# Kernel tuning notes

Hardware: AMD Instinct MI355X
Metric: run time of the kernel (lower is better)

## Reference

```python
import jax, jax.numpy as jnp
import numpy as np

IN_DIMS = 4
DEPTH = 4
C = IN_DIMS + 1                     # channels after time augmentation
SIG = sum(C ** k for k in range(1, DEPTH + 1))  # 780
N, T = 64, 1024


def setup_inputs() -> dict:
    key = jax.random.key(0)
    k1, k2, k3, k4, k5 = jax.random.split(key, 5)
    batch = jax.random.normal(k1, (N, T, IN_DIMS), dtype=jnp.float32)
    s_c = 1.0 / np.sqrt(C)
    conv_w = jax.random.normal(k2, (C, C), dtype=jnp.float32) * s_c
    conv_b = jax.random.normal(k3, (C,), dtype=jnp.float32) * s_c
    s_l = 1.0 / np.sqrt(SIG)
    lin_w = jax.random.normal(k4, (SIG, SIG), dtype=jnp.float32) * s_l
    lin_b = jax.random.normal(k5, (SIG,), dtype=jnp.float32) * s_l
    return {"batch": batch, "conv_w": conv_w, "conv_b": conv_b,
            "lin_w": lin_w, "lin_b": lin_b}


def _stream_signature(path):
    """Streamed path signature with zero basepoint.

    path: (n, t, C). Returns (n, t, SIG) where entry t is the signature of
    the piecewise-linear path (0, path[0], ..., path[t]) truncated at DEPTH,
    levels flattened in lexicographic (row-major) order like signatory.
    """
    n = path.shape[0]
    # increments; basepoint=True means first increment is path[:,0] - 0
    dx = jnp.concatenate([path[:, :1, :], path[:, 1:, :] - path[:, :-1, :]], axis=1)
    init = tuple(jnp.zeros((n, C ** k), path.dtype) for k in range(1, DEPTH + 1))

    def step(levels, d):
        # exp(d) in the truncated tensor algebra: e_k = d^{(x)k} / k!
        e = [d]
        for k in range(2, DEPTH + 1):
            e.append((jnp.einsum('na,nb->nab', e[-1], d) / k).reshape(n, -1))
        # Chen: new_k = e_k + S_k + sum_{i=1}^{k-1} S_i (x) e_{k-i}
        new = []
        for k in range(1, DEPTH + 1):
            acc = levels[k - 1] + e[k - 1]
            for i in range(1, k):
                acc = acc + jnp.einsum('na,nb->nab', levels[i - 1], e[k - i - 1]).reshape(n, -1)
            new.append(acc)
        new = tuple(new)
        return new, jnp.concatenate(new, axis=-1)

    _, ys = jax.lax.scan(step, init, jnp.swapaxes(dx, 0, 1))  # ys: (t, n, SIG)
    return jnp.swapaxes(ys, 0, 1)


def reference(batch, conv_w, conv_b, lin_w, lin_b):
    n, t, _ = batch.shape
    # time augmentation: append channel arange(1,T+1)/T
    time = (jnp.arange(1, t + 1, dtype=batch.dtype) / t)[None, :, None]
    a = jnp.concatenate([batch, jnp.broadcast_to(time, (n, t, 1))], axis=-1)  # (n,t,C)
    # kernel-size-1 conv1d == pointwise linear over channels
    b = a @ conv_w.T + conv_b                                                  # (n,t,C)
    c = _stream_signature(b)                                                   # (n,t,SIG)
    # zero out the first stream entry (torch.concat of zeros with c[:,1:,:])
    c = jnp.concatenate([jnp.zeros((n, 1, SIG), c.dtype), c[:, 1:, :]], axis=1)
    return jnp.tanh(c @ lin_w.T + lin_b)
```

## Files before the change

### kernel.cpp

```cpp
#include <hip/hip_runtime.h>
#include <math.h>

#define N_B 64
#define T_LEN 1024
#define IN_D 4
#define CH 5
#define SIG 780
#define KP 800
#define SEG_LEN 16
#define N_SEG 64
#define SC_L1 1.0f
#define SC_L2 0.25f
#define SC_L3 0.0625f
#define SC_L4 0.015625f

typedef _Float16 f16x8 __attribute__((ext_vector_type(8)));
typedef float f32x4 __attribute__((ext_vector_type(4)));

typedef __attribute__((address_space(1))) const void* as1cp;
typedef __attribute__((address_space(3))) void* as3p;

#define VMCNT(n) asm volatile("s_waitcnt vmcnt(" #n ")" ::: "memory")

__device__ __forceinline__ float fast_tanh(float x) {
  float ax = fabsf(x);
  float e = __expf(-2.0f * ax);
  float r = (1.0f - e) * __builtin_amdgcn_rcpf(1.0f + e);
  return copysignf(r, x);
}

__global__ __launch_bounds__(256) void conv_kernel(
    const float* __restrict__ batch,
    const float* __restrict__ conv_w,
    const float* __restrict__ conv_b,
    float* __restrict__ b_out) {
  int idx = blockIdx.x * blockDim.x + threadIdx.x;
  if (idx >= N_B * T_LEN) return;
  int t = idx & (T_LEN - 1);
  const float* a = batch + (size_t)idx * IN_D;
  float a0 = a[0], a1 = a[1], a2 = a[2], a3 = a[3];
  float tm = (float)(t + 1) / (float)T_LEN;
  float* o = b_out + (size_t)idx * CH;
#pragma unroll
  for (int j = 0; j < CH; ++j) {
    const float* w = conv_w + j * CH;
    float r = conv_b[j];
    r = fmaf(tm, w[4], r);
    r = fmaf(a3, w[3], r);
    r = fmaf(a2, w[2], r);
    r = fmaf(a1, w[1], r);
    r = fmaf(a0, w[0], r);
    o[j] = r;
  }
}

__global__ __launch_bounds__(320) void seg_kernel(
    const float* __restrict__ batch,
    const float* __restrict__ conv_w,
    const float* __restrict__ conv_b,
    float* __restrict__ P) {
  int s = blockIdx.x;
  int n = blockIdx.y;
  int tid = threadIdx.x;

  __shared__ float S[2][SIG];
  __shared__ float bc[(SEG_LEN + 1) * CH];
  __shared__ float dsh[SEG_LEN][CH];

  for (int i = tid; i < SIG; i += 320) S[0][i] = 0.0f;
  if (tid < (SEG_LEN + 1) * CH) {
    int r = s * SEG_LEN - 1 + tid / CH, ch = tid % CH;
    float v = 0.0f;
    if (r >= 0) {
      const float* a = batch + ((size_t)n * T_LEN + r) * IN_D;
      const float* w = conv_w + ch * CH;
      v = conv_b[ch];
      v = fmaf(a[0], w[0], v);
      v = fmaf(a[1], w[1], v);
      v = fmaf(a[2], w[2], v);
      v = fmaf(a[3], w[3], v);
      v = fmaf((float)(r + 1) * (1.0f / T_LEN), w[4], v);
    }
    bc[tid] = v;
  }
  __syncthreads();
  if (tid < SEG_LEN * CH) {
    int j = tid / CH, ch = tid % CH;
    dsh[j][ch] = bc[(j + 1) * CH + ch] - bc[j * CH + ch];
  }

  const int x0 = tid;
  const int x1 = tid + 320;
  const bool has1 = (tid < 305);
  const int a0i = x0 / 125, b0i = (x0 / 25) % 5, c0i = (x0 / 5) % 5, d0i = x0 % 5;
  const int a1i = x1 / 125, b1i = (x1 / 25) % 5, c1i = (x1 / 5) % 5, d1i = x1 % 5;
  const int s2_0 = x0 / 25, s3_0 = x0 / 5;
  const int s2_1 = x1 / 25, s3_1 = x1 / 5;
  const bool hasL3 = (tid < 125);
  const int ya = tid / 25, yb = (tid / 5) % 5, yc = tid % 5;
  const bool hasL2 = (tid < 25);
  const int za = tid / 5, zb = tid % 5;
  const bool hasL1 = (tid < CH);
  __syncthreads();

  int c = 0;
  for (int j = 0; j < SEG_LEN; ++j) {
    const float* Sc = S[c];
    float* Sn = S[c ^ 1];
    float n4_0, n4_1 = 0.0f, n3 = 0.0f, n2 = 0.0f, n1 = 0.0f;
    {
      float tH = fmaf(0.25f, dsh[j][a0i], Sc[a0i]);
      tH = fmaf((1.0f / 3.0f) * dsh[j][b0i], tH, Sc[5 + s2_0]);
      tH = fmaf(0.5f * dsh[j][c0i], tH, Sc[30 + s3_0]);
      n4_0 = fmaf(dsh[j][d0i], tH, Sc[155 + x0]);
    }
    if (has1) {
      float tH = fmaf(0.25f, dsh[j][a1i], Sc[a1i]);
      tH = fmaf((1.0f / 3.0f) * dsh[j][b1i], tH, Sc[5 + s2_1]);
      tH = fmaf(0.5f * dsh[j][c1i], tH, Sc[30 + s3_1]);
      n4_1 = fmaf(dsh[j][d1i], tH, Sc[155 + x1]);
    }
    if (hasL3) {
      float tH = fmaf((1.0f / 3.0f), dsh[j][ya], Sc[ya]);
      tH = fmaf(0.5f * dsh[j][yb], tH, Sc[5 + ya * 5 + yb]);
      n3 = fmaf(dsh[j][yc], tH, Sc[30 + tid]);
    }
    if (hasL2) {
      float tH = fmaf(0.5f, dsh[j][za], Sc[za]);
      n2 = fmaf(dsh[j][zb], tH, Sc[5 + tid]);
    }
    if (hasL1) n1 = Sc[tid] + dsh[j][tid];
    Sn[155 + x0] = n4_0;
    if (has1) Sn[155 + x1] = n4_1;
    if (hasL3) Sn[30 + tid] = n3;
    if (hasL2) Sn[5 + tid] = n2;
    if (hasL1) Sn[tid] = n1;
    __syncthreads();
    c ^= 1;
  }

  float* Pr = P + ((size_t)n * N_SEG + s) * SIG;
  for (int i = tid; i < SIG; i += 320) Pr[i] = S[c][i];
}

__global__ __launch_bounds__(640) void prefix_kernel(float* __restrict__ P) {
  int n = blockIdx.x;
  int tid = threadIdx.x;
  __shared__ float A[2][SIG];
  __shared__ float Bs[SIG];

  float* Pn = P + (size_t)n * N_SEG * SIG;
  for (int i = tid; i < SIG; i += 640) A[0][i] = Pn[i];
  int i0 = tid, i1 = tid + 640;
  float r0 = 0.f, r1 = 0.f;
  if (i0 < SIG) r0 = Pn[SIG + i0];
  if (i1 < SIG) r1 = Pn[SIG + i1];

  const int e4 = tid;
  const int q4a = e4 / 125, r125 = e4 % 125, r25 = e4 % 25, r5 = e4 % 5;
  const int e4d5 = e4 / 5, e4d25 = e4 / 25;
  const int e3 = tid;
  const int e3a = e3 / 25, e3r25 = e3 % 25, e3r5 = e3 % 5, e3d5 = e3 / 5;
  const int e2 = tid - 125;
  const int e1 = tid - 150;

  int c = 0;
  for (int s = 1; s < N_SEG; ++s) {
    if (i0 < SIG) Bs[i0] = r0;
    if (i1 < SIG) Bs[i1] = r1;
    __syncthreads();
    if (s + 1 < N_SEG) {
      const float* Pnx = Pn + (size_t)(s + 1) * SIG;
      if (i0 < SIG) r0 = Pnx[i0];
      if (i1 < SIG) r1 = Pnx[i1];
    }
    const float* Ac = A[c];
    float* An = A[c ^ 1];
    float* Po = Pn + (size_t)s * SIG;
    if (tid < 625) {
      float v4 = Ac[155 + e4] + Bs[155 + e4];
      v4 = fmaf(Ac[30 + e4d5], Bs[r5], v4);
      v4 = fmaf(Ac[5 + e4d25], Bs[5 + r25], v4);
      v4 = fmaf(Ac[q4a], Bs[30 + r125], v4);
      An[155 + e4] = v4; Po[155 + e4] = v4;
    }
    if (tid < 125) {
      float v3 = Ac[30 + e3] + Bs[30 + e3];
      v3 = fmaf(Ac[5 + e3d5], Bs[e3r5], v3);
      v3 = fmaf(Ac[e3a], Bs[5 + e3r25], v3);
      An[30 + e3] = v3; Po[30 + e3] = v3;
    } else if (tid < 150) {
      float v2 = Ac[5 + e2] + Bs[5 + e2];
      v2 = fmaf(Ac[e2 / 5], Bs[e2 % 5], v2);
      An[5 + e2] = v2; Po[5 + e2] = v2;
    } else if (tid < 155) {
      float v1 = Ac[e1] + Bs[e1];
      An[e1] = v1; Po[e1] = v1;
    }
    c ^= 1;
  }
}

__global__ __launch_bounds__(320) void emit_kernel(
    const float* __restrict__ batch,
    const float* __restrict__ conv_w,
    const float* __restrict__ conv_b,
    const float* __restrict__ P,
    _Float16* __restrict__ c1,
    _Float16* __restrict__ c2) {
  int s = blockIdx.x;
  int n = blockIdx.y;
  int tid = threadIdx.x;

  __shared__ float S[2][SIG];
  __shared__ float bc[(SEG_LEN + 1) * CH];
  __shared__ float dsh[SEG_LEN][CH];
  __shared__ __align__(16) _Float16 row1[2][KP];
  __shared__ __align__(16) _Float16 row2[2][KP];

  if (s == 0) {
    for (int i = tid; i < SIG; i += 320) S[0][i] = 0.0f;
  } else {
    const float* Pr = P + ((size_t)n * N_SEG + (s - 1)) * SIG;
    for (int i = tid; i < SIG; i += 320) S[0][i] = Pr[i];
  }
  if (tid < (SEG_LEN + 1) * CH) {
    int r = s * SEG_LEN - 1 + tid / CH, ch = tid % CH;
    float v = 0.0f;
    if (r >= 0) {
      const float* a = batch + ((size_t)n * T_LEN + r) * IN_D;
      const float* w = conv_w + ch * CH;
      v = conv_b[ch];
      v = fmaf(a[0], w[0], v);
      v = fmaf(a[1], w[1], v);
      v = fmaf(a[2], w[2], v);
      v = fmaf(a[3], w[3], v);
      v = fmaf((float)(r + 1) * (1.0f / T_LEN), w[4], v);
    }
    bc[tid] = v;
  }
  if (tid < KP - SIG) {
    row1[0][SIG + tid] = (_Float16)0.0f;
    row1[1][SIG + tid] = (_Float16)0.0f;
    row2[0][SIG + tid] = (_Float16)0.0f;
    row2[1][SIG + tid] = (_Float16)0.0f;
  }
  __syncthreads();
  if (tid < SEG_LEN * CH) {
    int j = tid / CH, ch = tid % CH;
    dsh[j][ch] = bc[(j + 1) * CH + ch] - bc[j * CH + ch];
  }

  const int x0 = tid;
  const int x1 = tid + 320;
  const bool has1 = (tid < 305);
  const int a0i = x0 / 125, b0i = (x0 / 25) % 5, c0i = (x0 / 5) % 5, d0i = x0 % 5;
  const int a1i = x1 / 125, b1i = (x1 / 25) % 5, c1i = (x1 / 5) % 5, d1i = x1 % 5;
  const int s2_0 = x0 / 25, s3_0 = x0 / 5;
  const int s2_1 = x1 / 25, s3_1 = x1 / 5;
  const bool hasL3 = (tid < 125);
  const int ya = tid / 25, yb = (tid / 5) % 5, yc = tid % 5;
  const bool hasL2 = (tid < 25);
  const int za = tid / 5, zb = tid % 5;
  const bool hasL1 = (tid < CH);
  __syncthreads();

  int c = 0;
  for (int j = 0; j < SEG_LEN; ++j) {
    int t = s * SEG_LEN + j;
    const float* Sc = S[c];
    float* Sn = S[c ^ 1];
    float n4_0, n4_1 = 0.0f, n3 = 0.0f, n2 = 0.0f, n1 = 0.0f;
    {
      float tH = fmaf(0.25f, dsh[j][a0i], Sc[a0i]);
      tH = fmaf((1.0f / 3.0f) * dsh[j][b0i], tH, Sc[5 + s2_0]);
      tH = fmaf(0.5f * dsh[j][c0i], tH, Sc[30 + s3_0]);
      n4_0 = fmaf(dsh[j][d0i], tH, Sc[155 + x0]);
    }
    if (has1) {
      float tH = fmaf(0.25f, dsh[j][a1i], Sc[a1i]);
      tH = fmaf((1.0f / 3.0f) * dsh[j][b1i], tH, Sc[5 + s2_1]);
      tH = fmaf(0.5f * dsh[j][c1i], tH, Sc[30 + s3_1]);
      n4_1 = fmaf(dsh[j][d1i], tH, Sc[155 + x1]);
    }
    if (hasL3) {
      float tH = fmaf((1.0f / 3.0f), dsh[j][ya], Sc[ya]);
      tH = fmaf(0.5f * dsh[j][yb], tH, Sc[5 + ya * 5 + yb]);
      n3 = fmaf(dsh[j][yc], tH, Sc[30 + tid]);
    }
    if (hasL2) {
      float tH = fmaf(0.5f, dsh[j][za], Sc[za]);
      n2 = fmaf(dsh[j][zb], tH, Sc[5 + tid]);
    }
    if (hasL1) n1 = Sc[tid] + dsh[j][tid];

    if (j > 0) {
      size_t base = ((size_t)n * T_LEN + (t - 1)) * KP;
      if (tid < 100) {
        *(float4*)(c1 + base + tid * 8) = *(const float4*)&row1[c][tid * 8];
      } else if (tid < 200) {
        int cc = tid - 100;
        *(float4*)(c2 + base + cc * 8) = *(const float4*)&row2[c][cc * 8];
      }
    }

    Sn[155 + x0] = n4_0;
    if (has1) Sn[155 + x1] = n4_1;
    if (hasL3) Sn[30 + tid] = n3;
    if (hasL2) Sn[5 + tid] = n2;
    if (hasL1) Sn[tid] = n1;

    float z = (t == 0) ? 0.0f : 1.0f;
    {
      float v = n4_0 * SC_L4 * z;
      _Float16 h = (_Float16)v;
      row1[c ^ 1][155 + x0] = h; row2[c ^ 1][155 + x0] = (_Float16)(v - (float)h);
    }
    if (has1) {
      float v = n4_1 * SC_L4 * z;
      _Float16 h = (_Float16)v;
      row1[c ^ 1][155 + x1] = h; row2[c ^ 1][155 + x1] = (_Float16)(v - (float)h);
    }
    if (hasL3) {
      float v = n3 * SC_L3 * z;
      _Float16 h = (_Float16)v;
      row1[c ^ 1][30 + tid] = h; row2[c ^ 1][30 + tid] = (_Float16)(v - (float)h);
    }
    if (hasL2) {
      float v = n2 * SC_L2 * z;
      _Float16 h = (_Float16)v;
      row1[c ^ 1][5 + tid] = h; row2[c ^ 1][5 + tid] = (_Float16)(v - (float)h);
    }
    if (hasL1) {
      float v = n1 * SC_L1 * z;
      _Float16 h = (_Float16)v;
      row1[c ^ 1][tid] = h; row2[c ^ 1][tid] = (_Float16)(v - (float)h);
    }
    __syncthreads();
    c ^= 1;
  }
  {
    size_t base = ((size_t)n * T_LEN + (s * SEG_LEN + SEG_LEN - 1)) * KP;
    if (tid < 100) {
      *(float4*)(c1 + base + tid * 8) = *(const float4*)&row1[c][tid * 8];
    } else if (tid < 200) {
      int cc = tid - 100;
      *(float4*)(c2 + base + cc * 8) = *(const float4*)&row2[c][cc * 8];
    }
  }
}

__global__ __launch_bounds__(256) void wconv_kernel(
    const float* __restrict__ W,
    _Float16* __restrict__ w1,
    _Float16* __restrict__ w2) {
  int idx = blockIdx.x * blockDim.x + threadIdx.x;
  if (idx >= 896 * KP) return;
  int nn = idx / KP, k = idx % KP;
  float v = 0.0f;
  if (nn < SIG && k < SIG) {
    float sc = (k < 5) ? 1.0f : (k < 30) ? 4.0f : (k < 155) ? 16.0f : 64.0f;
    v = W[(size_t)nn * SIG + k] * sc;
  }
  _Float16 h = (_Float16)v;
  w1[idx] = h;
  w2[idx] = (_Float16)(v - (float)h);
}

__global__ __launch_bounds__(512, 2) void gemm_mfma(
    const _Float16* __restrict__ A1p, const _Float16* __restrict__ A2p,
    const _Float16* __restrict__ B1p, const _Float16* __restrict__ B2p,
    const float* __restrict__ bias, float* __restrict__ out) {
  __shared__ _Float16 Al[3][2][256 * 32];
  __shared__ _Float16 Bl[3][2][128 * 32];

  int tid = threadIdx.x;
  int lane = tid & 63, wid = tid >> 6;
  int wm = wid >> 1, wn = wid & 1;

  int b = blockIdx.x;
  int xcd = b & 7, sidx = b >> 3;
  int mt = (sidx / 7) * 8 + xcd;
  int nt = sidx % 7;
  int m0 = mt * 256;
  int n0 = nt * 128;

  f32x4 acc[4][4];
#pragma unroll
  for (int i = 0; i < 4; ++i)
#pragma unroll
    for (int j = 0; j < 4; ++j) acc[i][j] = (f32x4){0.f, 0.f, 0.f, 0.f};

  int sr = lane >> 2, scn = lane & 3;
  int swst = (sr ^ (sr >> 2)) & 3;
  int qg = scn ^ swst;
  int fr = lane & 15, fq = lane >> 4;
  int swf = (fr ^ (fr >> 2)) & 3;
  int fchunk = fq ^ swf;

  auto stageA = [&](int kb, int buf, int i) {
    int k0 = kb * 32;
    int linear = wid * 4 + i;
    int plane = linear >> 4, grp = linear & 15;
    size_t g = (size_t)(m0 + grp * 16 + sr) * KP + k0 + qg * 8;
    const _Float16* src = (plane ? A2p : A1p) + g;
    __builtin_amdgcn_global_load_lds((as1cp)src, (as3p)(&Al[buf][plane][grp * 512]), 16, 0, 0);
  };
  auto stageB = [&](int kb, int buf, int i) {
    int k0 = kb * 32;
    int linear = wid * 2 + i;
    int plane = linear >> 3, grp = linear & 7;
    size_t g = (size_t)(n0 + grp * 16 + sr) * KP + k0 + qg * 8;
    const _Float16* src = (plane ? B2p : B1p) + g;
    __builtin_amdgcn_global_load_lds((as1cp)src, (as3p)(&Bl[buf][plane][grp * 512]), 16, 0, 0);
  };

#pragma unroll
  for (int i = 0; i < 4; ++i) stageA(0, 0, i);
#pragma unroll
  for (int i = 0; i < 2; ++i) stageB(0, 0, i);
#pragma unroll
  for (int i = 0; i < 4; ++i) stageA(1, 1, i);
#pragma unroll
  for (int i = 0; i < 2; ++i) stageB(1, 1, i);

  int cur = 0;
#pragma unroll 1
  for (int kb = 0; kb < 25; ++kb) {
    int nx = cur + 2; if (nx >= 3) nx -= 3;
    bool pf = (kb + 2 < 25);
    if (kb < 24) { VMCNT(6); } else { VMCNT(0); }
    __builtin_amdgcn_s_barrier();
    __builtin_amdgcn_sched_barrier(0);
    f16x8 a1f[4], a2f[4], b1f[4], b2f[4];
    {
      int off = (wn * 64 + 0 * 16 + fr) * 32 + fchunk * 8;
      b1f[0] = *(const f16x8*)&Bl[cur][0][off];
      b2f[0] = *(const f16x8*)&Bl[cur][1][off];
    }
#pragma unroll
    for (int tm = 0; tm < 4; ++tm) {
      int off = (wm * 64 + tm * 16 + fr) * 32 + fchunk * 8;
      a1f[tm] = *(const f16x8*)&Al[cur][0][off];
      a2f[tm] = *(const f16x8*)&Al[cur][1][off];
    }
#pragma unroll
    for (int tn = 1; tn < 4; ++tn) {
      int off = (wn * 64 + tn * 16 + fr) * 32 + fchunk * 8;
      b1f[tn] = *(const f16x8*)&Bl[cur][0][off];
      b2f[tn] = *(const f16x8*)&Bl[cur][1][off];
    }
    if (pf) {
      stageA(kb + 2, nx, 0); stageA(kb + 2, nx, 1);
      stageA(kb + 2, nx, 2); stageA(kb + 2, nx, 3);
      stageB(kb + 2, nx, 0); stageB(kb + 2, nx, 1);
    }
#pragma unroll
    for (int tn = 0; tn < 4; ++tn) {
#pragma unroll
      for (int tm = 0; tm < 4; ++tm) {
        acc[tm][tn] = __builtin_amdgcn_mfma_f32_16x16x32_f16(a1f[tm], b1f[tn], acc[tm][tn], 0, 0, 0);
        acc[tm][tn] = __builtin_amdgcn_mfma_f32_16x16x32_f16(a1f[tm], b2f[tn], acc[tm][tn], 0, 0, 0);
        acc[tm][tn] = __builtin_amdgcn_mfma_f32_16x16x32_f16(a2f[tm], b1f[tn], acc[tm][tn], 0, 0, 0);
      }
    }
    cur = cur + 1; if (cur >= 3) cur -= 3;
  }
  __syncthreads();

  float* ep = (float*)(&Al[0][0][0]) + wid * 2112;

  float bv[4];
#pragma unroll
  for (int tn = 0; tn < 4; ++tn) {
    int nn = n0 + wn * 64 + tn * 16 + fr;
    bv[tn] = (nn < SIG) ? bias[nn] : 0.0f;
  }
#pragma unroll
  for (int h = 0; h < 2; ++h) {
#pragma unroll
    for (int tm2 = 0; tm2 < 2; ++tm2) {
      int tm = h * 2 + tm2;
#pragma unroll
      for (int tn = 0; tn < 4; ++tn) {
#pragma unroll
        for (int r = 0; r < 4; ++r) {
          int lr = tm2 * 16 + fq * 4 + r;
          int lc = tn * 16 + fr;
          ep[lr * 66 + lc] = fast_tanh(acc[tm][tn][r] + bv[tn]);
        }
      }
    }
#pragma unroll
    for (int p = 0; p < 2; ++p) {
      int lr = lane & 31;
      int ck = (lane >> 5) * 2 + p;
      int gm = m0 + wm * 64 + h * 32 + lr;
      int gc0 = n0 + wn * 64 + ck * 16;
#pragma unroll
      for (int q = 0; q < 4; ++q) {
        int col = gc0 + q * 4;
        if (col + 3 < SIG) {
          *(float4*)(out + (size_t)gm * SIG + col) =
              *(const float4*)&ep[lr * 66 + ck * 16 + q * 4];
        } else if (col < SIG) {
#pragma unroll
          for (int e = 0; e < 4; ++e) {
            int c2 = col + e;
            if (c2 < SIG) out[(size_t)gm * SIG + c2] = ep[lr * 66 + ck * 16 + q * 4 + e];
          }
        }
      }
    }
  }
}

__global__ __launch_bounds__(320) void sig_kernel_fb(
    const float* __restrict__ b_in, float* __restrict__ c_out) {
  int n = blockIdx.x;
  int tid = threadIdx.x;
  __shared__ float S[SIG];
  __shared__ float bc[64 * CH];
  __shared__ float dsh[CH];
  __shared__ float pb[CH];
  for (int i = tid; i < SIG; i += 320) S[i] = 0.0f;
  if (tid < CH) pb[tid] = 0.0f;
  const float* bn = b_in + (size_t)n * T_LEN * CH;
  float* cn = c_out + (size_t)n * T_LEN * SIG;
  const int x0 = tid, x1 = tid + 320;
  const bool has1 = (tid < 305);
  const int a0i = x0 / 125, b0i = (x0 / 25) % 5, c0i = (x0 / 5) % 5, d0i = x0 % 5;
  const int a1i = x1 / 125, b1i = (x1 / 25) % 5, c1i = (x1 / 5) % 5, d1i = x1 % 5;
  const int s2_0 = x0 / 25, s3_0 = x0 / 5, s2_1 = x1 / 25, s3_1 = x1 / 5;
  const bool hasL3 = (tid < 125);
  const int ya = tid / 25, yb = (tid / 5) % 5, yc = tid % 5;
  const bool hasL2 = (tid < 25);
  const int za = tid / 5, zb = tid % 5;
  const bool hasL1 = (tid < CH);
  for (int t = 0; t < T_LEN; ++t) {
    if ((t & 63) == 0) {
      __syncthreads();
      bc[tid] = bn[t * CH + tid];
      __syncthreads();
    }
    if (tid < CH) {
      float cur = bc[(t & 63) * CH + tid];
      dsh[tid] = cur - pb[tid];
      pb[tid] = cur;
    }
    __syncthreads();
    float n4_0, n4_1 = 0.0f, n3 = 0.0f, n2 = 0.0f, n1 = 0.0f;
    {
      float tH = fmaf(0.25f, dsh[a0i], S[a0i]);
      tH = fmaf((1.0f / 3.0f) * dsh[b0i], tH, S[5 + s2_0]);
      tH = fmaf(0.5f * dsh[c0i], tH, S[30 + s3_0]);
      n4_0 = fmaf(dsh[d0i], tH, S[155 + x0]);
    }
    if (has1) {
      float tH = fmaf(0.25f, dsh[a1i], S[a1i]);
      tH = fmaf((1.0f / 3.0f) * dsh[b1i], tH, S[5 + s2_1]);
      tH = fmaf(0.5f * dsh[c1i], tH, S[30 + s3_1]);
      n4_1 = fmaf(dsh[d1i], tH, S[155 + x1]);
    }
    if (hasL3) {
      float tH = fmaf((1.0f / 3.0f), dsh[ya], S[ya]);
      tH = fmaf(0.5f * dsh[yb], tH, S[5 + ya * 5 + yb]);
      n3 = fmaf(dsh[yc], tH, S[30 + tid]);
    }
    if (hasL2) {
      float tH = fmaf(0.5f, dsh[za], S[za]);
      n2 = fmaf(dsh[zb], tH, S[5 + tid]);
    }
    if (hasL1) n1 = S[tid] + dsh[tid];
    __syncthreads();
    S[155 + x0] = n4_0;
    if (has1) S[155 + x1] = n4_1;
    if (hasL3) S[30 + tid] = n3;
    if (hasL2) S[5 + tid] = n2;
    if (hasL1) S[tid] = n1;
    float* crow = cn + (size_t)t * SIG;
    float z = (t == 0) ? 0.0f : 1.0f;
    crow[155 + x0] = n4_0 * z;
    if (has1) crow[155 + x1] = n4_1 * z;
    if (hasL3) crow[30 + tid] = n3 * z;
    if (hasL2) crow[5 + tid] = n2 * z;
    if (hasL1) crow[tid] = n1 * z;
    __syncthreads();
  }
}

#define BM 256
#define BN 64
#define BK 16
__global__ __launch_bounds__(256) void gemm_tanh_fb(
    const float* __restrict__ Cmat, const float* __restrict__ W,
    const float* __restrict__ bias, float* __restrict__ out) {
  __shared__ float As[BK][BM + 4];
  __shared__ float Ws[BK][BN + 4];
  int tid = threadIdx.x;
  int tx = tid & 7, ty = tid >> 3;
  int m0 = blockIdx.x * BM, n0 = blockIdx.y * BN;
  float acc[8][8];
#pragma unroll
  for (int i = 0; i < 8; ++i)
#pragma unroll
    for (int j = 0; j < 8; ++j) acc[i][j] = 0.0f;
  for (int kb = 0; kb < SIG; kb += BK) {
    __syncthreads();
#pragma unroll
    for (int p = 0; p < 4; ++p) {
      int id = tid + p * 256;
      int row = id >> 2, kg = (id & 3) * 4, gk = kb + kg;
      float4 v = make_float4(0.f, 0.f, 0.f, 0.f);
      if (gk < SIG) v = *(const float4*)(Cmat + (size_t)(m0 + row) * SIG + gk);
      As[kg + 0][row] = v.x; As[kg + 1][row] = v.y;
      As[kg + 2][row] = v.z; As[kg + 3][row] = v.w;
    }
    {
      int row = tid >> 2, kg = (tid & 3) * 4, gk = kb + kg, wr = n0 + row;
      float4 v = make_float4(0.f, 0.f, 0.f, 0.f);
      if (gk < SIG && wr < SIG) v = *(const float4*)(W + (size_t)wr * SIG + gk);
      Ws[kg + 0][row] = v.x; Ws[kg + 1][row] = v.y;
      Ws[kg + 2][row] = v.z; Ws[kg + 3][row] = v.w;
    }
    __syncthreads();
#pragma unroll
    for (int k = 0; k < BK; ++k) {
      float af[8], wf[8];
      *(float4*)&af[0] = *(const float4*)&As[k][ty * 8];
      *(float4*)&af[4] = *(const float4*)&As[k][ty * 8 + 4];
      *(float4*)&wf[0] = *(const float4*)&Ws[k][tx * 8];
      *(float4*)&wf[4] = *(const float4*)&Ws[k][tx * 8 + 4];
#pragma unroll
      for (int i = 0; i < 8; ++i)
#pragma unroll
        for (int j = 0; j < 8; ++j) acc[i][j] = fmaf(af[i], wf[j], acc[i][j]);
    }
  }
#pragma unroll
  for (int i = 0; i < 8; ++i) {
    int m = m0 + ty * 8 + i;
    float* orow = out + (size_t)m * SIG;
#pragma unroll
    for (int jj = 0; jj < 8; jj += 4) {
      int col = n0 + tx * 8 + jj;
      if (col < SIG) {
        float4 r;
        r.x = tanhf(acc[i][jj + 0] + bias[col + 0]);
        r.y = tanhf(acc[i][jj + 1] + bias[col + 1]);
        r.z = tanhf(acc[i][jj + 2] + bias[col + 2]);
        r.w = tanhf(acc[i][jj + 3] + bias[col + 3]);
        *(float4*)(orow + col) = r;
      }
    }
  }
}

extern "C" void kernel_launch(void* const* d_in, const int* in_sizes, int n_in,
                              void* d_out, int out_size, void* d_ws, size_t ws_size,
                              hipStream_t stream) {
  const float* batch = (const float*)d_in[0];
  const float* conv_w = (const float*)d_in[1];
  const float* conv_b = (const float*)d_in[2];
  const float* lin_w = (const float*)d_in[3];
  const float* lin_b = (const float*)d_in[4];
  float* out = (float*)d_out;

  const size_t plane_elems = (size_t)N_B * T_LEN * KP;
  const size_t wplane_elems = (size_t)896 * KP;
  const size_t P_elems = (size_t)N_B * N_SEG * SIG;
  const size_t bp_elems = (size_t)N_B * T_LEN * CH;
  const size_t need_big = 2 * plane_elems * sizeof(_Float16) +
                          2 * wplane_elems * sizeof(_Float16) +
                          P_elems * sizeof(float);

  if (ws_size >= need_big) {
    _Float16* c1 = (_Float16*)d_ws;
    _Float16* c2 = c1 + plane_elems;
    _Float16* w1 = c2 + plane_elems;
    _Float16* w2 = w1 + wplane_elems;
    float* P = (float*)(w2 + wplane_elems);

    wconv_kernel<<<dim3((896 * KP + 255) / 256), dim3(256), 0, stream>>>(
        lin_w, w1, w2);
    seg_kernel<<<dim3(N_SEG, N_B), dim3(320), 0, stream>>>(batch, conv_w, conv_b, P);
    prefix_kernel<<<dim3(N_B), dim3(640), 0, stream>>>(P);
    emit_kernel<<<dim3(N_SEG, N_B), dim3(320), 0, stream>>>(
        batch, conv_w, conv_b, P, c1, c2);
    gemm_mfma<<<dim3(1792), dim3(512), 0, stream>>>(c1, c2, w1, w2, lin_b, out);
  } else {
    float* b_path = (float*)d_ws;
    float* c_sig = (float*)d_ws + bp_elems;
    conv_kernel<<<dim3((N_B * T_LEN + 255) / 256), dim3(256), 0, stream>>>(
        batch, conv_w, conv_b, b_path);
    sig_kernel_fb<<<dim3(N_B), dim3(320), 0, stream>>>(b_path, c_sig);
    gemm_tanh_fb<<<dim3((N_B * T_LEN) / BM, (SIG + BN - 1) / BN), dim3(256), 0, stream>>>(
        c_sig, lin_w, lin_b, out);
  }
}
```

Before: 630.3 us.

## Software-pipeline LDS fragment reads one k-block ahead of the MFMA loop

Restructures the GEMM main loop so that the A/B fragment reads from LDS for the next k-block are issued right after the MFMAs for each tile column. The aim is to hide LDS read latency behind matrix-core work. Fragment offsets are hoisted, a prologue loads the first block, and an epilogue runs the final MFMAs. In exchange, the wait now drains all outstanding global-to-LDS loads every iteration (vmcnt 0 instead of 6). That shortens the effective global prefetch slack and could expose global-memory latency.

```diff
diff --git a/kernel.cpp b/kernel.cpp
--- a/kernel.cpp
+++ b/kernel.cpp
@@ -424,36 +424,40 @@
 #pragma unroll
   for (int i = 0; i < 2; ++i) stageB(1, 1, i);
 
-  int cur = 0;
+  f16x8 a1f[4], a2f[4], b1f[4], b2f[4];
+
+  int aoff[4], boff[4];
+#pragma unroll
+  for (int tm = 0; tm < 4; ++tm)
+    aoff[tm] = (wm * 64 + tm * 16 + fr) * 32 + fchunk * 8;
+#pragma unroll
+  for (int tn = 0; tn < 4; ++tn)
+    boff[tn] = (wn * 64 + tn * 16 + fr) * 32 + fchunk * 8;
+
+  VMCNT(6);
+  __builtin_amdgcn_s_barrier();
+  __builtin_amdgcn_sched_barrier(0);
+#pragma unroll
+  for (int tn = 0; tn < 4; ++tn) {
+    b1f[tn] = *(const f16x8*)&Bl[0][0][boff[tn]];
+    b2f[tn] = *(const f16x8*)&Bl[0][1][boff[tn]];
+  }
+#pragma unroll
+  for (int tm = 0; tm < 4; ++tm) {
+    a1f[tm] = *(const f16x8*)&Al[0][0][aoff[tm]];
+    a2f[tm] = *(const f16x8*)&Al[0][1][aoff[tm]];
+  }
+
+  int rb = 1, sb = 2;
 #pragma unroll 1
-  for (int kb = 0; kb < 25; ++kb) {
-    int nx = cur + 2; if (nx >= 3) nx -= 3;
-    bool pf = (kb + 2 < 25);
-    if (kb < 24) { VMCNT(6); } else { VMCNT(0); }
+  for (int kb = 0; kb < 24; ++kb) {
+    VMCNT(0);
     __builtin_amdgcn_s_barrier();
     __builtin_amdgcn_sched_barrier(0);
-    f16x8 a1f[4], a2f[4], b1f[4], b2f[4];
-    {
-      int off = (wn * 64 + 0 * 16 + fr) * 32 + fchunk * 8;
-      b1f[0] = *(const f16x8*)&Bl[cur][0][off];
-      b2f[0] = *(const f16x8*)&Bl[cur][1][off];
-    }
-#pragma unroll
-    for (int tm = 0; tm < 4; ++tm) {
-      int off = (wm * 64 + tm * 16 + fr) * 32 + fchunk * 8;
-      a1f[tm] = *(const f16x8*)&Al[cur][0][off];
-      a2f[tm] = *(const f16x8*)&Al[cur][1][off];
-    }
-#pragma unroll
-    for (int tn = 1; tn < 4; ++tn) {
-      int off = (wn * 64 + tn * 16 + fr) * 32 + fchunk * 8;
-      b1f[tn] = *(const f16x8*)&Bl[cur][0][off];
-      b2f[tn] = *(const f16x8*)&Bl[cur][1][off];
-    }
-    if (pf) {
-      stageA(kb + 2, nx, 0); stageA(kb + 2, nx, 1);
-      stageA(kb + 2, nx, 2); stageA(kb + 2, nx, 3);
-      stageB(kb + 2, nx, 0); stageB(kb + 2, nx, 1);
+    if (kb + 2 < 25) {
+      stageA(kb + 2, sb, 0); stageA(kb + 2, sb, 1);
+      stageA(kb + 2, sb, 2); stageA(kb + 2, sb, 3);
+      stageB(kb + 2, sb, 0); stageB(kb + 2, sb, 1);
     }
 #pragma unroll
     for (int tn = 0; tn < 4; ++tn) {
@@ -463,8 +467,25 @@
         acc[tm][tn] = __builtin_amdgcn_mfma_f32_16x16x32_f16(a1f[tm], b2f[tn], acc[tm][tn], 0, 0, 0);
         acc[tm][tn] = __builtin_amdgcn_mfma_f32_16x16x32_f16(a2f[tm], b1f[tn], acc[tm][tn], 0, 0, 0);
       }
-    }
-    cur = cur + 1; if (cur >= 3) cur -= 3;
+      b1f[tn] = *(const f16x8*)&Bl[rb][0][boff[tn]];
+      b2f[tn] = *(const f16x8*)&Bl[rb][1][boff[tn]];
+    }
+#pragma unroll
+    for (int tm = 0; tm < 4; ++tm) {
+      a1f[tm] = *(const f16x8*)&Al[rb][0][aoff[tm]];
+      a2f[tm] = *(const f16x8*)&Al[rb][1][aoff[tm]];
+    }
+    rb = rb + 1; if (rb == 3) rb = 0;
+    sb = sb + 1; if (sb == 3) sb = 0;
+  }
+#pragma unroll
+  for (int tn = 0; tn < 4; ++tn) {
+#pragma unroll
+    for (int tm = 0; tm < 4; ++tm) {
+      acc[tm][tn] = __builtin_amdgcn_mfma_f32_16x16x32_f16(a1f[tm], b1f[tn], acc[tm][tn], 0, 0, 0);
+      acc[tm][tn] = __builtin_amdgcn_mfma_f32_16x16x32_f16(a1f[tm], b2f[tn], acc[tm][tn], 0, 0, 0);
+      acc[tm][tn] = __builtin_amdgcn_mfma_f32_16x16x32_f16(a2f[tm], b1f[tn], acc[tm][tn], 0, 0, 0);
+    }
   }
   __syncthreads();
 
```

New measurement: 713.9 us. 13.3% more time.

## Split GEMM into wide 256x256-tile kernel plus narrow tail kernel

Applied to the files above, without the earlier changes.

Replaces the single 256x128-tile GEMM, with its triple-buffered LDS, by two launches. The first uses 256x256 tiles with double buffering to cover columns 0-767. The second reuses the old 128-wide kernel for the remaining column tile starting at 768. The wider tile doubles A-operand reuse per block and cuts redundant A loads and block count. In exchange it uses more accumulator registers, which may spill or hurt occupancy, drops a pipeline stage, and adds an extra kernel launch.

```diff
diff --git a/kernel.cpp b/kernel.cpp
--- a/kernel.cpp
+++ b/kernel.cpp
@@ -367,7 +367,154 @@
   w2[idx] = (_Float16)(v - (float)h);
 }
 
-__global__ __launch_bounds__(512, 2) void gemm_mfma(
+__global__ __launch_bounds__(512, 2) void gemm_mfma_w(
+    const _Float16* __restrict__ A1p, const _Float16* __restrict__ A2p,
+    const _Float16* __restrict__ B1p, const _Float16* __restrict__ B2p,
+    const float* __restrict__ bias, float* __restrict__ out) {
+  __shared__ _Float16 Al[2][2][256 * 32];
+  __shared__ _Float16 Bl[2][2][256 * 32];
+
+  int tid = threadIdx.x;
+  int lane = tid & 63, wid = tid >> 6;
+  int wm = wid >> 1, wn = wid & 1;
+
+  int b = blockIdx.x;
+  int xcd = b & 7, sidx = b >> 3;
+  int mt = (sidx / 3) * 8 + xcd;
+  int nt = sidx % 3;
+  int m0 = mt * 256;
+  int n0 = nt * 256;
+
+  f32x4 acc[4][8];
+#pragma unroll
+  for (int i = 0; i < 4; ++i)
+#pragma unroll
+    for (int j = 0; j < 8; ++j) acc[i][j] = (f32x4){0.f, 0.f, 0.f, 0.f};
+
+  int sr = lane >> 2, scn = lane & 3;
+  int swst = (sr ^ (sr >> 2)) & 3;
+  int qg = scn ^ swst;
+  int fr = lane & 15, fq = lane >> 4;
+  int swf = (fr ^ (fr >> 2)) & 3;
+  int fchunk = fq ^ swf;
+
+  auto stageA = [&](int kb, int buf, int i) {
+    int k0 = kb * 32;
+    int linear = wid * 4 + i;
+    int plane = linear >> 4, grp = linear & 15;
+    size_t g = (size_t)(m0 + grp * 16 + sr) * KP + k0 + qg * 8;
+    const _Float16* src = (plane ? A2p : A1p) + g;
+    __builtin_amdgcn_global_load_lds((as1cp)src, (as3p)(&Al[buf][plane][grp * 512]), 16, 0, 0);
+  };
+  auto stageB = [&](int kb, int buf, int i) {
+    int k0 = kb * 32;
+    int linear = wid * 4 + i;
+    int plane = linear >> 4, grp = linear & 15;
+    size_t g = (size_t)(n0 + grp * 16 + sr) * KP + k0 + qg * 8;
+    const _Float16* src = (plane ? B2p : B1p) + g;
+    __builtin_amdgcn_global_load_lds((as1cp)src, (as3p)(&Bl[buf][plane][grp * 512]), 16, 0, 0);
+  };
+
+#pragma unroll
+  for (int i = 0; i < 4; ++i) stageA(0, 0, i);
+#pragma unroll
+  for (int i = 0; i < 4; ++i) stageB(0, 0, i);
+
+  int cur = 0;
+#pragma unroll 1
+  for (int kb = 0; kb < 25; ++kb) {
+    VMCNT(0);
+    __builtin_amdgcn_s_barrier();
+    __builtin_amdgcn_sched_barrier(0);
+    f16x8 a1f[4], a2f[4], b1f[8], b2f[8];
+    {
+      int off = (wn * 128 + fr) * 32 + fchunk * 8;
+      b1f[0] = *(const f16x8*)&Bl[cur][0][off];
+      b2f[0] = *(const f16x8*)&Bl[cur][1][off];
+    }
+#pragma unroll
+    for (int tm = 0; tm < 4; ++tm) {
+      int off = (wm * 64 + tm * 16 + fr) * 32 + fchunk * 8;
+      a1f[tm] = *(const f16x8*)&Al[cur][0][off];
+      a2f[tm] = *(const f16x8*)&Al[cur][1][off];
+    }
+#pragma unroll
+    for (int tn = 1; tn < 8; ++tn) {
+      int off = (wn * 128 + tn * 16 + fr) * 32 + fchunk * 8;
+      b1f[tn] = *(const f16x8*)&Bl[cur][0][off];
+      b2f[tn] = *(const f16x8*)&Bl[cur][1][off];
+    }
+    if (kb + 1 < 25) {
+#pragma unroll
+      for (int i = 0; i < 4; ++i) stageA(kb + 1, cur ^ 1, i);
+#pragma unroll
+      for (int i = 0; i < 4; ++i) stageB(kb + 1, cur ^ 1, i);
+    }
+#pragma unroll
+    for (int tn = 0; tn < 8; ++tn) {
+#pragma unroll
+      for (int tm = 0; tm < 4; ++tm) {
+        acc[tm][tn] = __builtin_amdgcn_mfma_f32_16x16x32_f16(a1f[tm], b1f[tn], acc[tm][tn], 0, 0, 0);
+        acc[tm][tn] = __builtin_amdgcn_mfma_f32_16x16x32_f16(a1f[tm], b2f[tn], acc[tm][tn], 0, 0, 0);
+        acc[tm][tn] = __builtin_amdgcn_mfma_f32_16x16x32_f16(a2f[tm], b1f[tn], acc[tm][tn], 0, 0, 0);
+      }
+    }
+    cur ^= 1;
+  }
+  __syncthreads();
+
+  float* ep = ((wid < 4) ? (float*)&Al[0][0][0] : (float*)&Bl[0][0][0]) +
+              (wid & 3) * 2112;
+
+#pragma unroll
+  for (int nh = 0; nh < 2; ++nh) {
+    float bv[4];
+#pragma unroll
+    for (int tn = 0; tn < 4; ++tn) {
+      int nn = n0 + wn * 128 + nh * 64 + tn * 16 + fr;
+      bv[tn] = (nn < SIG) ? bias[nn] : 0.0f;
+    }
+#pragma unroll
+    for (int h = 0; h < 2; ++h) {
+#pragma unroll
+      for (int tm2 = 0; tm2 < 2; ++tm2) {
+        int tm = h * 2 + tm2;
+#pragma unroll
+        for (int tn = 0; tn < 4; ++tn) {
+#pragma unroll
+          for (int r = 0; r < 4; ++r) {
+            int lr = tm2 * 16 + fq * 4 + r;
+            int lc = tn * 16 + fr;
+            ep[lr * 66 + lc] = fast_tanh(acc[tm][nh * 4 + tn][r] + bv[tn]);
+          }
+        }
+      }
+#pragma unroll
+      for (int p = 0; p < 2; ++p) {
+        int lr = lane & 31;
+        int ck = (lane >> 5) * 2 + p;
+        int gm = m0 + wm * 64 + h * 32 + lr;
+        int gc0 = n0 + wn * 128 + nh * 64 + ck * 16;
+#pragma unroll
+        for (int q = 0; q < 4; ++q) {
+          int col = gc0 + q * 4;
+          if (col + 3 < SIG) {
+            *(float4*)(out + (size_t)gm * SIG + col) =
+                *(const float4*)&ep[lr * 66 + ck * 16 + q * 4];
+          } else if (col < SIG) {
+#pragma unroll
+            for (int e = 0; e < 4; ++e) {
+              int c2 = col + e;
+              if (c2 < SIG) out[(size_t)gm * SIG + c2] = ep[lr * 66 + ck * 16 + q * 4 + e];
+            }
+          }
+        }
+      }
+    }
+  }
+}
+
+__global__ __launch_bounds__(512, 2) void gemm_mfma_n(
     const _Float16* __restrict__ A1p, const _Float16* __restrict__ A2p,
     const _Float16* __restrict__ B1p, const _Float16* __restrict__ B2p,
     const float* __restrict__ bias, float* __restrict__ out) {
@@ -379,11 +526,10 @@
   int wm = wid >> 1, wn = wid & 1;
 
   int b = blockIdx.x;
-  int xcd = b & 7, sidx = b >> 3;
-  int mt = (sidx / 7) * 8 + xcd;
-  int nt = sidx % 7;
+  int xcd = b & 7;
+  int mt = (b >> 3) * 8 + xcd;
   int m0 = mt * 256;
-  int n0 = nt * 128;
+  int n0 = 768;
 
   f32x4 acc[4][4];
 #pragma unroll
@@ -687,7 +833,8 @@
     prefix_kernel<<<dim3(N_B), dim3(640), 0, stream>>>(P);
     emit_kernel<<<dim3(N_SEG, N_B), dim3(320), 0, stream>>>(
         batch, conv_w, conv_b, P, c1, c2);
-    gemm_mfma<<<dim3(1792), dim3(512), 0, stream>>>(c1, c2, w1, w2, lin_b, out);
+    gemm_mfma_w<<<dim3(768), dim3(512), 0, stream>>>(c1, c2, w1, w2, lin_b, out);
+    gemm_mfma_n<<<dim3(256), dim3(512), 0, stream>>>(c1, c2, w1, w2, lin_b, out);
   } else {
     float* b_path = (float*)d_ws;
     float* c_sig = (float*)d_ws + bp_elems;
```

New measurement: 656.7 us. 1.04x slower.
